# Kernel optimization log

Hardware: AMD Instinct MI355X
Metric: run time of the kernel (lower is better)

Reference implementation:

```python
import jax, jax.numpy as jnp
import numpy as np
from jax import lax

HID = 2048; NK = 16; NV = 32; DK = 128; DV = 128; KSZ = 4; CHUNK = 64; S = 2048
KEY_DIM = NK * DK; VAL_DIM = NV * DV; CONV_DIM = 2 * KEY_DIM + VAL_DIM
EPS = 1e-6


def l2norm(x, eps=1e-6):
    return x * lax.rsqrt((x * x).sum(-1, keepdims=True) + eps)


def chunk_gated_delta_rule(q, k, v, g, beta, chunk=CHUNK):
    # q,k: [B,S,Hv,DK]; v: [B,S,Hv,DV]; g,beta: [B,S,Hv]
    q = l2norm(q); k = l2norm(k)  # use_qk_l2norm_in_kernel=True
    q, k, v = (jnp.swapaxes(x, 1, 2) for x in (q, k, v))  # [B,H,S,D]
    g = jnp.swapaxes(g, 1, 2); beta = jnp.swapaxes(beta, 1, 2)  # [B,H,S]
    B, H, Ssz, Dk = k.shape; Dv = v.shape[-1]
    N = Ssz // chunk  # seq_len chosen divisible by chunk -> pad is no-op
    q = q * (Dk ** -0.5)
    vb = v * beta[..., None]
    kb = k * beta[..., None]
    rs = lambda x: x.reshape(B, H, N, chunk, x.shape[-1])
    q, k, v, kb, vb = map(rs, (q, k, v, kb, vb))
    g = jnp.cumsum(g.reshape(B, H, N, chunk), axis=-1)
    tril = jnp.tril(jnp.ones((chunk, chunk), bool))
    stril = jnp.tril(jnp.ones((chunk, chunk), bool), -1)
    diff = jnp.where(tril, g[..., :, None] - g[..., None, :], 0.0)
    decay_mask = jnp.where(tril, jnp.exp(diff), 0.0)  # [B,H,N,C,C]
    attn = jnp.where(stril, -(kb @ jnp.swapaxes(k, -1, -2)) * decay_mask, 0.0)
    # UT (WY) transform: sequential row updates, scan over in-chunk index
    def ut_body(a, i):
        row = jnp.take(a, i, axis=-2)  # [B,H,N,C]
        new = row + jnp.einsum('bhnk,bhnkj->bhnj', row, a)
        return a.at[:, :, :, i, :].set(new), None
    attn, _ = lax.scan(ut_body, attn, jnp.arange(1, chunk))
    attn = attn + jnp.eye(chunk, dtype=attn.dtype)
    u = attn @ vb                                   # [B,H,N,C,DV]
    kcd = attn @ (kb * jnp.exp(g)[..., None])       # [B,H,N,C,DK]
    init = jnp.zeros((B, H, Dk, Dv), q.dtype)
    def step(state, inp):
        q_i, k_i, u_i, kcd_i, g_i, dm_i = inp
        scores = (q_i @ jnp.swapaxes(k_i, -1, -2)) * dm_i
        v_new = u_i - kcd_i @ state
        inter = (q_i * jnp.exp(g_i)[..., None]) @ state
        o = inter + scores @ v_new
        gl = g_i[..., -1]  # [B,H]
        state = state * jnp.exp(gl)[..., None, None] + jnp.einsum(
            'bhcd,bhce->bhde', k_i * jnp.exp(gl[..., None] - g_i)[..., None], v_new)
        return state, o
    mv = lambda x: jnp.moveaxis(x, 2, 0)
    _, out = lax.scan(step, init, (mv(q), mv(k), mv(u), mv(kcd), mv(g), mv(decay_mask)))
    out = jnp.moveaxis(out, 0, 2).reshape(B, H, Ssz, Dv)
    return jnp.swapaxes(out, 1, 2)  # [B,S,H,DV]


def setup_inputs() -> dict:
    key = jax.random.key(0)
    ks = jax.random.split(key, 8)
    return {
        'hidden_states': jax.random.normal(ks[0], (S, HID), jnp.float32),
        'W_qkv': jax.random.normal(ks[1], (CONV_DIM, HID), jnp.float32) * 0.02,
        'W_z': jax.random.normal(ks[2], (VAL_DIM, HID), jnp.float32) * 0.02,
        'W_a': jax.random.normal(ks[3], (NV, HID), jnp.float32) * 0.02,
        'W_b': jax.random.normal(ks[4], (NV, HID), jnp.float32) * 0.02,
        'conv_w': jax.random.normal(ks[5], (CONV_DIM, 1, KSZ), jnp.float32) * 0.1,
        'dt_bias': jnp.ones((NV,), jnp.float32),
        'A_log': jnp.log(jax.random.uniform(ks[6], (NV,), jnp.float32, 0.1, 16.0)),
        'norm_w': jnp.ones((DV,), jnp.float32),
        'W_out': jax.random.normal(ks[7], (HID, VAL_DIM), jnp.float32) * 0.02,
    }


def reference(hidden_states, W_qkv, W_z, W_a, W_b, conv_w, dt_bias, A_log, norm_w, W_out):
    x = hidden_states  # [S, HID]
    mixed = x @ W_qkv.T  # [S, CONV_DIM]
    z = (x @ W_z.T).reshape(-1, DV)  # [S*NV, DV]
    a = x @ W_a.T  # [S, NV]
    b = x @ W_b.T
    # causal depthwise conv1d (torch pads K-1 both sides then slices [:S])
    conv = lax.conv_general_dilated(
        mixed.T[None], conv_w, (1,), [(KSZ - 1, 0)],
        dimension_numbers=('NCH', 'OIH', 'NCH'), feature_group_count=CONV_DIM)
    mixed = jax.nn.silu(conv[0].T)  # [S, CONV_DIM]
    q = mixed[:, :KEY_DIM].reshape(1, S, NK, DK)
    k = mixed[:, KEY_DIM:2 * KEY_DIM].reshape(1, S, NK, DK)
    v = mixed[:, 2 * KEY_DIM:].reshape(1, S, NV, DV)
    beta = jax.nn.sigmoid(b)[None]  # [1,S,NV]
    g = (-jnp.exp(A_log) * jax.nn.softplus(a + dt_bias))[None]  # [1,S,NV]
    ratio = NV // NK
    q = jnp.repeat(q, ratio, axis=2)
    k = jnp.repeat(k, ratio, axis=2)
    core = chunk_gated_delta_rule(q, k, v, g, beta)  # [1,S,NV,DV]
    h = core.reshape(-1, DV)  # [S*NV, DV]
    var = jnp.mean(h * h, axis=-1, keepdims=True)
    h = h * lax.rsqrt(var + EPS) * norm_w
    h = h * jax.nn.silu(z)
    out = h.reshape(S, VAL_DIM) @ W_out.T  # [S, HID]
    return out
```

## Files before the change

### kernel.cpp

```cpp
#include <hip/hip_runtime.h>
#include <hip/hip_bf16.h>
#include <math.h>

#define S_LEN   2048
#define HIDDIM  2048
#define NKH     16
#define NVH     32
#define DKD     128
#define DVD     128
#define CCH     64
#define NCHK    32
#define KEY_DIM 2048
#define VAL_DIM 4096
#define CONV_DIM 8192

#define PA_LDS_BYTES (16384 + 16384 + 32768 + 4096 + 4096 + 256 + 256 + 256)
#define PB_LDS_BYTES ((8192+8192+4096+8192+2048+1024+1024)*2 + 64*4)
#define G256_LDS_BYTES (3 * 24576 * 2)
#define G128_LDS_BYTES (3 * 16384 * 2)

typedef __bf16 bf16x8 __attribute__((ext_vector_type(8)));
typedef float f32x4 __attribute__((ext_vector_type(4)));

__device__ __forceinline__ float sigmoid_f(float x) { return 1.f / (1.f + __expf(-x)); }
__device__ __forceinline__ float silu_f(float x) { return x * sigmoid_f(x); }
__device__ __forceinline__ ushort f2bf(float f) {
    unsigned u = __float_as_uint(f);
    u += 0x7fffu + ((u >> 16) & 1u);
    return (ushort)(u >> 16);
}
__device__ __forceinline__ float bf2f(ushort u) {
    return __uint_as_float((unsigned)u << 16);
}

#define GLL(srcp, dstp) __builtin_amdgcn_global_load_lds( \
    (const __attribute__((address_space(1))) void*)(srcp), \
    (__attribute__((address_space(3))) void*)(dstp), 16, 0, 0)

__global__ __launch_bounds__(256) void cast_kernel(
    const float* __restrict__ in, ushort* __restrict__ out, int n8)
{
    int t = blockIdx.x * 256 + threadIdx.x;
    if (t >= n8) return;
    float4 v0 = *(const float4*)(in + (size_t)t * 8);
    float4 v1 = *(const float4*)(in + (size_t)t * 8 + 4);
    union { ushort u[8]; uint4 v; } r;
    r.u[0] = f2bf(v0.x); r.u[1] = f2bf(v0.y); r.u[2] = f2bf(v0.z); r.u[3] = f2bf(v0.w);
    r.u[4] = f2bf(v1.x); r.u[5] = f2bf(v1.y); r.u[6] = f2bf(v1.z); r.u[7] = f2bf(v1.w);
    *(uint4*)(out + (size_t)t * 8) = r.v;
}

__global__ __launch_bounds__(256) void cast_ab_kernel(
    const float* __restrict__ Wa, const float* __restrict__ Wb, ushort* __restrict__ out)
{
    int t = blockIdx.x * 256 + threadIdx.x;
    int row = t >> 8;
    int c8 = (t & 255) * 8;
    union { ushort u[8]; uint4 v; } r;
    if (row < 64) {
        const float* src = (row < 32) ? (Wa + (size_t)row * HIDDIM + c8)
                                      : (Wb + (size_t)(row - 32) * HIDDIM + c8);
        float4 v0 = *(const float4*)(src);
        float4 v1 = *(const float4*)(src + 4);
        r.u[0] = f2bf(v0.x); r.u[1] = f2bf(v0.y); r.u[2] = f2bf(v0.z); r.u[3] = f2bf(v0.w);
        r.u[4] = f2bf(v1.x); r.u[5] = f2bf(v1.y); r.u[6] = f2bf(v1.z); r.u[7] = f2bf(v1.w);
    } else {
        r.u[0] = r.u[1] = r.u[2] = r.u[3] = r.u[4] = r.u[5] = r.u[6] = r.u[7] = 0;
    }
    *(uint4*)(out + (size_t)t * 8) = r.v;
}

__global__ __launch_bounds__(512, 2) void gemm256_kernel(
    const ushort* __restrict__ A, const ushort* __restrict__ B,
    float* __restrict__ C0, float* __restrict__ C1,
    int K, int NSPLIT, int ldc0, int ldc1)
{
    extern __shared__ ushort g2s[];
    const int tid = threadIdx.x;
    const int wv = tid >> 6, ln = tid & 63;
    const int wm = wv >> 2, wn = wv & 3;
    const int lrow = ln & 15, lkg = ln >> 4;
    const int bm = blockIdx.y * 128, bn = blockIdx.x * 256;

    int soffA[2], soffB[4];
#pragma unroll
    for (int j = 0; j < 4; ++j) {
        int g = tid + j * 512;
        int frag = g >> 7, ks = (g >> 6) & 1, l = g & 63;
        int off = (frag * 16 + (l & 15)) * K + ks * 32 + (l >> 4) * 8;
        if (j < 2) soffA[j] = off;
        soffB[j] = off;
    }
    const ushort* Abase = A + (size_t)bm * K;
    const ushort* Bbase = B + (size_t)bn * K;

    f32x4 acc[4][4];
#pragma unroll
    for (int m = 0; m < 4; ++m)
#pragma unroll
        for (int n = 0; n < 4; ++n) {
            f32x4 z = {0.f, 0.f, 0.f, 0.f};
            acc[m][n] = z;
        }

#define G256_STAGE(bb, k0) do {                                            \
        ushort* bufA_ = g2s + (bb) * 24576;                                \
        ushort* bufB_ = bufA_ + 8192;                                      \
        _Pragma("unroll")                                                  \
        for (int j_ = 0; j_ < 2; ++j_)                                     \
            GLL(Abase + soffA[j_] + (k0), bufA_ + (j_ * 512 + wv * 64) * 8);\
        _Pragma("unroll")                                                  \
        for (int j_ = 0; j_ < 4; ++j_)                                     \
            GLL(Bbase + soffB[j_] + (k0), bufB_ + (j_ * 512 + wv * 64) * 8);\
    } while (0)

    const int T = K >> 6;
    G256_STAGE(0, 0);
    G256_STAGE(1, 64);
    int bb = 0;
    for (int t = 0; t < T; ++t) {
        if (t + 1 < T) {
            asm volatile("s_waitcnt vmcnt(6)" ::: "memory");
        } else {
            asm volatile("s_waitcnt vmcnt(0)" ::: "memory");
        }
        __builtin_amdgcn_s_barrier();
        if (t + 2 < T) G256_STAGE((bb >= 1) ? (bb - 1) : (bb + 2), (t + 2) * 64);
        const ushort* LA = g2s + bb * 24576;
        const ushort* LB = LA + 8192;
        __builtin_amdgcn_s_setprio(1);
#pragma unroll
        for (int ks = 0; ks < 2; ++ks) {
            bf16x8 afv[4], bfv[4];
#pragma unroll
            for (int mf = 0; mf < 4; ++mf)
                afv[mf] = *(const bf16x8*)&LA[(((wm * 4 + mf) * 2 + ks) * 64 + ln) * 8];
#pragma unroll
            for (int nf = 0; nf < 4; ++nf)
                bfv[nf] = *(const bf16x8*)&LB[(((wn * 4 + nf) * 2 + ks) * 64 + ln) * 8];
#pragma unroll
            for (int mf = 0; mf < 4; ++mf)
#pragma unroll
                for (int nf = 0; nf < 4; ++nf)
                    acc[mf][nf] = __builtin_amdgcn_mfma_f32_16x16x32_bf16(
                        afv[mf], bfv[nf], acc[mf][nf], 0, 0, 0);
        }
        __builtin_amdgcn_s_setprio(0);
        bb = (bb == 2) ? 0 : bb + 1;
    }
#undef G256_STAGE

    const bool inC1 = (bn >= NSPLIT);
    float* Cp = inC1 ? C1 : C0;
    const int ldc = inC1 ? ldc1 : ldc0;
    const int cb = bn + wn * 64 - (inC1 ? NSPLIT : 0);
#pragma unroll
    for (int mf = 0; mf < 4; ++mf) {
        const int row0 = bm + wm * 64 + mf * 16 + lkg * 4;
#pragma unroll
        for (int nf = 0; nf < 4; ++nf) {
            float* cp = Cp + (size_t)row0 * ldc + cb + nf * 16 + lrow;
#pragma unroll
            for (int j = 0; j < 4; ++j) cp[(size_t)j * ldc] = acc[mf][nf][j];
        }
    }
}

__global__ __launch_bounds__(256, 2) void gemm128_kernel(
    const ushort* __restrict__ A, const ushort* __restrict__ B,
    float* __restrict__ C, int N, int K)
{
    extern __shared__ ushort g1s[];
    const int tid = threadIdx.x;
    const int wv = tid >> 6, ln = tid & 63;
    const int wm = wv >> 1, wn = wv & 1;
    const int lrow = ln & 15, lkg = ln >> 4;
    const int bm = blockIdx.y * 128, bn = blockIdx.x * 128;

    int soff[4];
#pragma unroll
    for (int j = 0; j < 4; ++j) {
        int g = tid + j * 256;
        int frag = g >> 7, ks = (g >> 6) & 1, l = g & 63;
        soff[j] = (frag * 16 + (l & 15)) * K + ks * 32 + (l >> 4) * 8;
    }
    const ushort* Abase = A + (size_t)bm * K;
    const ushort* Bbase = B + (size_t)bn * K;

    f32x4 acc[4][4];
#pragma unroll
    for (int m = 0; m < 4; ++m)
#pragma unroll
        for (int n = 0; n < 4; ++n) {
            f32x4 z = {0.f, 0.f, 0.f, 0.f};
            acc[m][n] = z;
        }

#define G128_STAGE(bb, k0) do {                                            \
        ushort* bufA_ = g1s + (bb) * 16384;                                \
        ushort* bufB_ = bufA_ + 8192;                                      \
        _Pragma("unroll")                                                  \
        for (int j_ = 0; j_ < 4; ++j_) {                                   \
            GLL(Abase + soff[j_] + (k0), bufA_ + (j_ * 256 + wv * 64) * 8);\
            GLL(Bbase + soff[j_] + (k0), bufB_ + (j_ * 256 + wv * 64) * 8);\
        }                                                                  \
    } while (0)

    const int T = K >> 6;
    G128_STAGE(0, 0);
    G128_STAGE(1, 64);
    int bb = 0;
    for (int t = 0; t < T; ++t) {
        if (t + 1 < T) {
            asm volatile("s_waitcnt vmcnt(8)" ::: "memory");
        } else {
            asm volatile("s_waitcnt vmcnt(0)" ::: "memory");
        }
        __builtin_amdgcn_s_barrier();
        if (t + 2 < T) G128_STAGE((bb >= 1) ? (bb - 1) : (bb + 2), (t + 2) * 64);
        const ushort* LA = g1s + bb * 16384;
        const ushort* LB = LA + 8192;
        __builtin_amdgcn_s_setprio(1);
#pragma unroll
        for (int ks = 0; ks < 2; ++ks) {
            bf16x8 afv[4], bfv[4];
#pragma unroll
            for (int mf = 0; mf < 4; ++mf)
                afv[mf] = *(const bf16x8*)&LA[(((wm * 4 + mf) * 2 + ks) * 64 + ln) * 8];
#pragma unroll
            for (int nf = 0; nf < 4; ++nf)
                bfv[nf] = *(const bf16x8*)&LB[(((wn * 4 + nf) * 2 + ks) * 64 + ln) * 8];
#pragma unroll
            for (int mf = 0; mf < 4; ++mf)
#pragma unroll
                for (int nf = 0; nf < 4; ++nf)
                    acc[mf][nf] = __builtin_amdgcn_mfma_f32_16x16x32_bf16(
                        afv[mf], bfv[nf], acc[mf][nf], 0, 0, 0);
        }
        __builtin_amdgcn_s_setprio(0);
        bb = (bb == 2) ? 0 : bb + 1;
    }
#undef G128_STAGE

#pragma unroll
    for (int mf = 0; mf < 4; ++mf) {
        const int row0 = bm + wm * 64 + mf * 16 + lkg * 4;
#pragma unroll
        for (int nf = 0; nf < 4; ++nf) {
            float* cp = C + (size_t)row0 * N + bn + wn * 64 + nf * 16 + lrow;
#pragma unroll
            for (int j = 0; j < 4; ++j) cp[(size_t)j * N] = acc[mf][nf][j];
        }
    }
}

__global__ __launch_bounds__(256) void conv_silu_kernel(
    const float* __restrict__ pre, const float* __restrict__ cw, float* __restrict__ out)
{
    int idx = blockIdx.x * 256 + threadIdx.x;
    const int NC4 = CONV_DIM / 4;
    int s = idx / NC4;
    int c = (idx % NC4) * 4;
    float w[4][4];
#pragma unroll
    for (int j = 0; j < 4; ++j) {
        float4 wj = *(const float4*)(cw + (size_t)(c + j) * 4);
        w[j][0] = wj.x; w[j][1] = wj.y; w[j][2] = wj.z; w[j][3] = wj.w;
    }
    float acc[4] = {0.f, 0.f, 0.f, 0.f};
#pragma unroll
    for (int t = 0; t < 4; ++t) {
        int ss = s - 3 + t;
        if (ss >= 0) {
            float4 x = *(const float4*)(pre + (size_t)ss * CONV_DIM + c);
            acc[0] = fmaf(x.x, w[0][t], acc[0]);
            acc[1] = fmaf(x.y, w[1][t], acc[1]);
            acc[2] = fmaf(x.z, w[2][t], acc[2]);
            acc[3] = fmaf(x.w, w[3][t], acc[3]);
        }
    }
    float4 o = make_float4(silu_f(acc[0]), silu_f(acc[1]), silu_f(acc[2]), silu_f(acc[3]));
    *(float4*)(out + (size_t)s * CONV_DIM + c) = o;
}

__global__ __launch_bounds__(256) void gb_kernel(
    const float* __restrict__ ab, const float* __restrict__ dt_bias,
    const float* __restrict__ A_log, float* __restrict__ g, float* __restrict__ beta)
{
    int idx = blockIdx.x * 256 + threadIdx.x;
    int s = idx >> 5, h = idx & 31;
    float av = ab[(size_t)s * 128 + h] + dt_bias[h];
    float sp = (av > 20.f) ? av : log1pf(__expf(av));
    g[idx] = -__expf(A_log[h]) * sp;
    beta[idx] = sigmoid_f(ab[(size_t)s * 128 + 32 + h]);
}

__global__ __launch_bounds__(256) void l2norm_kernel(
    const float* __restrict__ mixed, ushort* __restrict__ qnb, float* __restrict__ kn)
{
    int gw = (blockIdx.x * 256 + threadIdx.x) >> 6;
    int lane = threadIdx.x & 63;
    int isk = gw >= S_LEN * NKH;
    int r = gw - isk * S_LEN * NKH;
    int s = r / NKH, kh = r % NKH;
    const float* src = mixed + (size_t)s * CONV_DIM + isk * KEY_DIM + kh * DKD;
    float2 x = *(const float2*)(src + lane * 2);
    float ss = x.x * x.x + x.y * x.y;
#pragma unroll
    for (int m = 1; m < 64; m <<= 1) ss += __shfl_xor(ss, m, 64);
    float scale = rsqrtf(ss + 1e-6f);
    if (!isk) {
        scale *= 0.08838834764831843f;
        union { ushort u[2]; uint v; } p;
        p.u[0] = f2bf(x.x * scale); p.u[1] = f2bf(x.y * scale);
        *(uint*)(qnb + ((size_t)(s * NKH + kh)) * DKD + lane * 2) = p.v;
    } else {
        float* dst = kn + ((size_t)(s * NKH + kh)) * DKD + lane * 2;
        *(float2*)dst = make_float2(x.x * scale, x.y * scale);
    }
}

__global__ __launch_bounds__(256) void phaseA_kernel(
    const ushort* __restrict__ qnb, const float* __restrict__ kn,
    const float* __restrict__ mixed, const float* __restrict__ gbuf,
    const float* __restrict__ betabuf,
    float* __restrict__ u, ushort* __restrict__ kcd,
    ushort* __restrict__ scores, float* __restrict__ gcs_out,
    ushort* __restrict__ knT)
{
    extern __shared__ char pasm[];
    ushort* kb    = (ushort*)(pasm);
    ushort* qb    = (ushort*)(pasm + 16384);
    ushort* Xb    = (ushort*)(pasm + 32768);
    float*  Adiag = (float*)(pasm + 65536);
    ushort* Ab    = (ushort*)(pasm + 69632);
    float*  gcs_s = (float*)(pasm + 73728);
    float*  bet_s = (float*)(pasm + 73984);
    float*  scK_s = (float*)(pasm + 74240);
    float*  Pf    = (float*)qb;

    const int n = blockIdx.x, h = blockIdx.y, kh = h >> 1;
    const int tid = threadIdx.x;
    const int s0 = n * CCH;
    const int wv = tid >> 6, ln = tid & 63;
    const int lrow = ln & 15, lkg = ln >> 4;

    float xr[64];
    if (tid < 128) {
        const float* vp = mixed + (size_t)s0 * CONV_DIM + 2 * KEY_DIM + h * DVD + tid;
#pragma unroll
        for (int i = 0; i < 64; ++i) xr[i] = vp[(size_t)i * CONV_DIM];
    } else {
        const float* kp = kn + ((size_t)s0 * NKH + kh) * DKD + (tid - 128);
#pragma unroll
        for (int i = 0; i < 64; ++i) xr[i] = kp[(size_t)i * (NKH * DKD)];
    }

    {
        uint4 z = {0, 0, 0, 0};
#pragma unroll
        for (int i = 0; i < 8; ++i)
            *(uint4*)&Xb[(i * 256 + tid) * 8] = z;
        *(uint4*)&Ab[tid * 8] = z;
    }

    if (tid < 64) {
        float gv = gbuf[(size_t)(s0 + tid) * NVH + h];
#pragma unroll
        for (int off = 1; off < 64; off <<= 1) {
            float pv = __shfl_up(gv, off, 64);
            if (tid >= off) gv += pv;
        }
        float bv = betabuf[(size_t)(s0 + tid) * NVH + h];
        gcs_s[tid] = gv;
        bet_s[tid] = bv;
        scK_s[tid] = bv * __expf(gv);
        gcs_out[(size_t)h * S_LEN + s0 + tid] = gv;
    }

    {
        const int r = tid >> 2, c0 = (tid & 3) * 32;
        const int mbase = (((r >> 4) * 4 + (tid & 3)) * 64 + (r & 15)) * 8;
        const float* ksrc = kn + ((size_t)(s0 + r) * NKH + kh) * DKD + c0;
#pragma unroll
        for (int j0 = 0; j0 < 4; ++j0) {
            float4 v0 = *(const float4*)(ksrc + j0 * 8);
            float4 v1 = *(const float4*)(ksrc + j0 * 8 + 4);
            union { ushort us[8]; uint4 v; } p;
            p.us[0] = f2bf(v0.x); p.us[1] = f2bf(v0.y); p.us[2] = f2bf(v0.z); p.us[3] = f2bf(v0.w);
            p.us[4] = f2bf(v1.x); p.us[5] = f2bf(v1.y); p.us[6] = f2bf(v1.z); p.us[7] = f2bf(v1.w);
            *(uint4*)&kb[mbase + (j0 << 7)] = p.v;
        }
        const ushort* qsrc = qnb + ((size_t)(s0 + r) * NKH + kh) * DKD + c0;
#pragma unroll
        for (int j0 = 0; j0 < 4; ++j0) {
            uint4 v = *(const uint4*)(qsrc + j0 * 8);
            *(uint4*)&qb[mbase + (j0 << 7)] = v;
        }
    }
    __syncthreads();

    f32x4 accA[4], accQ[4];
#pragma unroll
    for (int j = 0; j < 4; ++j) {
        f32x4 z = {0.f, 0.f, 0.f, 0.f};
        accA[j] = z; accQ[j] = z;
    }
#pragma unroll
    for (int ks = 0; ks < 4; ++ks) {
        bf16x8 a_k = *(const bf16x8*)&kb[((wv * 4 + ks) * 64 + ln) * 8];
        bf16x8 a_q = *(const bf16x8*)&qb[((wv * 4 + ks) * 64 + ln) * 8];
#pragma unroll
        for (int j = 0; j < 4; ++j) {
            bf16x8 b_k = *(const bf16x8*)&kb[((j * 4 + ks) * 64 + ln) * 8];
            accA[j] = __builtin_amdgcn_mfma_f32_16x16x32_bf16(a_k, b_k, accA[j], 0, 0, 0);
            accQ[j] = __builtin_amdgcn_mfma_f32_16x16x32_bf16(a_q, b_k, accQ[j], 0, 0, 0);
        }
    }
    {
        ushort* scp = scores + (size_t)(h * NCHK + n) * (CCH * CCH);
#pragma unroll
        for (int j = 0; j < 4; ++j) {
            const int c = j * 16 + lrow;
            const float gc = gcs_s[c];
#pragma unroll
            for (int jj = 0; jj < 4; ++jj) {
                const int i = wv * 16 + lkg * 4 + jj;
                const float e = __expf(gcs_s[i] - gc);
                float sv = (i >= c) ? (accQ[j][jj] * e) : 0.f;
                scp[i * CCH + c] = f2bf(sv);
                float aval = (i > c) ? (-bet_s[i] * accA[j][jj] * e) : 0.f;
                if (j == wv) {
                    Adiag[wv * 256 + (i & 15) * 16 + lrow] = aval;
                } else if (j < wv) {
                    const int f = (wv == 1) ? 0 : ((wv == 2) ? 1 : (2 + (j >> 1)));
                    const int lk = ((j & 1) << 4) | lrow;
                    const int lane2 = (i & 15) | ((lk >> 3) << 4);
                    Ab[(f * 64 + lane2) * 8 + (lk & 7)] = f2bf(aval);
                }
            }
        }
    }
    if (tid < 128) {
#pragma unroll
        for (int i4 = 0; i4 < 16; ++i4) {
            float4 b4 = *(const float4*)&bet_s[i4 * 4];
            xr[i4 * 4 + 0] *= b4.x; xr[i4 * 4 + 1] *= b4.y;
            xr[i4 * 4 + 2] *= b4.z; xr[i4 * 4 + 3] *= b4.w;
        }
    } else {
#pragma unroll
        for (int i4 = 0; i4 < 16; ++i4) {
            float4 b4 = *(const float4*)&scK_s[i4 * 4];
            xr[i4 * 4 + 0] *= b4.x; xr[i4 * 4 + 1] *= b4.y;
            xr[i4 * 4 + 2] *= b4.z; xr[i4 * 4 + 3] *= b4.w;
        }
    }
    __syncthreads();

    const int ct = tid >> 4, lct = tid & 15;
#pragma unroll
    for (int s = 0; s < 4; ++s) {
        float y[16];
        float pr[16];
        if (s > 0) {
#pragma unroll
            for (int r = 0; r < 16; ++r) pr[r] = Pf[r * 256 + tid];
        } else {
#pragma unroll
            for (int r = 0; r < 16; ++r) pr[r] = 0.f;
        }
#pragma unroll
        for (int r = 0; r < 16; ++r) {
            float acc = xr[s * 16 + r] + pr[r];
#pragma unroll
            for (int k4 = 0; k4 < 16; k4 += 4) {
                if (k4 < r) {
                    float4 a4 = *(const float4*)&Adiag[s * 256 + r * 16 + k4];
                    if (k4 + 0 < r) acc = fmaf(a4.x, y[k4 + 0], acc);
                    if (k4 + 1 < r) acc = fmaf(a4.y, y[k4 + 1], acc);
                    if (k4 + 2 < r) acc = fmaf(a4.z, y[k4 + 2], acc);
                    if (k4 + 3 < r) acc = fmaf(a4.w, y[k4 + 3], acc);
                }
            }
            y[r] = acc;
        }
        if (tid < 128) {
            float* up = u + (size_t)(h * NCHK + n) * (CCH * DVD) + (s * 16) * DVD + tid;
#pragma unroll
            for (int r = 0; r < 16; ++r) up[r * DVD] = y[r];
        } else {
            ushort* kp = kcd + (size_t)(h * NCHK + n) * (CCH * DKD) + (s * 16) * DKD + (tid - 128);
#pragma unroll
            for (int r = 0; r < 16; ++r) kp[r * DKD] = f2bf(y[r]);
        }
        if (s < 3) {
#pragma unroll
            for (int half = 0; half < 2; ++half) {
                union { ushort us[8]; uint4 v; } p;
#pragma unroll
                for (int e = 0; e < 8; ++e) p.us[e] = f2bf(y[half * 8 + e]);
                const int kg = (s & 1) * 2 + half;
                *(uint4*)&Xb[(((s >> 1) * 16 + ct) * 64 + (kg * 16 + lct)) * 8] = p.v;
            }
            __syncthreads();
            const int snx = s + 1;
            const int nT2 = (snx + 1) >> 1;
            f32x4 accP[4];
#pragma unroll
            for (int ctl = 0; ctl < 4; ++ctl) {
                f32x4 z = {0.f, 0.f, 0.f, 0.f};
                accP[ctl] = z;
            }
#pragma unroll
            for (int t2 = 0; t2 < 2; ++t2) {
                if (t2 < nT2) {
                    const int f = (snx == 1) ? 0 : ((snx == 2) ? 1 : (2 + t2));
                    bf16x8 a = *(const bf16x8*)&Ab[(f * 64 + ln) * 8];
#pragma unroll
                    for (int ctl = 0; ctl < 4; ++ctl) {
                        bf16x8 b = *(const bf16x8*)&Xb[((t2 * 16 + wv * 4 + ctl) * 64 + ln) * 8];
                        accP[ctl] = __builtin_amdgcn_mfma_f32_16x16x32_bf16(a, b, accP[ctl], 0, 0, 0);
                    }
                }
            }
#pragma unroll
            for (int ctl = 0; ctl < 4; ++ctl)
#pragma unroll
                for (int jj = 0; jj < 4; ++jj)
                    Pf[(lkg * 4 + jj) * 256 + wv * 64 + ctl * 16 + lrow] = accP[ctl][jj];
            __syncthreads();
        }
    }

    if (!(h & 1)) {
        const int dk = tid >> 1, ch = (tid & 1) * 32;
        ushort* dst = knT + ((size_t)(kh * NCHK + n) * DKD + dk) * CCH + ch;
        const int kpart = ((dk >> 5) * 64) * 8 + (((dk >> 3) & 3) << 4) * 8 + (dk & 7);
#pragma unroll
        for (int j0 = 0; j0 < 32; j0 += 8) {
            union { ushort us[8]; uint4 v; } p;
#pragma unroll
            for (int j = 0; j < 8; ++j) {
                const int row = ch + j0 + j;
                p.us[j] = kb[((row >> 4) * 4 * 64 + (row & 15)) * 8 + kpart];
            }
            *(uint4*)(dst + j0) = p.v;
        }
    }
}

__global__ __launch_bounds__(256) void phaseB_kernel(
    const ushort* __restrict__ qnb, const ushort* __restrict__ knT,
    const float* __restrict__ u, const ushort* __restrict__ kcd,
    const ushort* __restrict__ sc, const float* __restrict__ gcs,
    float* __restrict__ obuf)
{
    extern __shared__ ushort smu[];
    ushort* qorg  = smu;
    ushort* kcorg = smu + 8192;
    ushort* scorg = smu + 16384;
    ushort* kTorg = smu + 20480;
    ushort* storg = smu + 28672;
    ushort* vnorg = smu + 30720;
    ushort* vnsorg= smu + 31744;
    float* gcs_s  = (float*)(smu + 32768);

    const int h = blockIdx.x;
    const int dvb = blockIdx.y;
    const int d0 = dvb * 16;
    const int kh = h >> 1;
    const int tid = threadIdx.x;
    const int wv = tid >> 6, ln = tid & 63;
    const int lrow = ln & 15, lkg = ln >> 4;

    for (int i = tid; i < 2048 / 8; i += 256) {
        uint4 z = {0, 0, 0, 0};
        *(uint4*)&storg[i * 8] = z;
    }

    const int q_lane  = lrow * (NKH * DKD) + kh * DKD + wv * 32 + lkg * 8;
    const int kc_lane = lrow * DKD + wv * 32 + lkg * 8;
    const int st_lane = ((tid >> 7) * 16 + lrow) * 64 + ((tid >> 6) & 1) * 32 + lkg * 8;
    const int dst_e   = wv * 512;

    f32x4 accS0 = {0.f, 0.f, 0.f, 0.f}, accS1 = {0.f, 0.f, 0.f, 0.f};

    for (int n = 0; n < NCHK; ++n) {
        const int s0 = n * CCH;
        const ushort* qsrc  = qnb + (size_t)s0 * (NKH * DKD);
        const ushort* kcsrc = kcd + (size_t)(h * NCHK + n) * (CCH * DKD);
        const ushort* scsrc = sc  + (size_t)(h * NCHK + n) * (CCH * CCH);
        const ushort* kTsrc = knT + (size_t)(kh * NCHK + n) * (DKD * CCH);
#pragma unroll
        for (int r = 0; r < 4; ++r) {
            GLL(qsrc + q_lane + r * 32768, &qorg[r * 2048 + dst_e]);
            GLL(kcsrc + kc_lane + r * 2048, &kcorg[r * 2048 + dst_e]);
            GLL(kTsrc + st_lane + r * 2048, &kTorg[r * 2048 + dst_e]);
        }
#pragma unroll
        for (int r = 0; r < 2; ++r)
            GLL(scsrc + st_lane + r * 2048, &scorg[r * 2048 + dst_e]);
        if (tid < 64) gcs_s[tid] = gcs[(size_t)h * S_LEN + s0 + tid];
        __syncthreads();

        f32x4 accv = {0.f, 0.f, 0.f, 0.f};
        f32x4 acco = {0.f, 0.f, 0.f, 0.f};
#pragma unroll
        for (int ks = 0; ks < 4; ++ks) {
            bf16x8 b_st = *(const bf16x8*)&storg[(ks * 64 + ln) * 8];
            bf16x8 a_kc = *(const bf16x8*)&kcorg[((wv * 4 + ks) * 64 + ln) * 8];
            bf16x8 a_q  = *(const bf16x8*)&qorg[((wv * 4 + ks) * 64 + ln) * 8];
            accv = __builtin_amdgcn_mfma_f32_16x16x32_bf16(a_kc, b_st, accv, 0, 0, 0);
            acco = __builtin_amdgcn_mfma_f32_16x16x32_bf16(a_q, b_st, acco, 0, 0, 0);
        }
        const float* up = u + (size_t)(h * NCHK + n) * (CCH * DVD)
                            + (wv * 16 + lkg * 4) * DVD + d0 + lrow;
        float u0 = up[0], u1 = up[DVD], u2 = up[2 * DVD], u3 = up[3 * DVD];
        const float gl = gcs_s[63];
        float vn0 = u0 - accv[0], vn1 = u1 - accv[1];
        float vn2 = u2 - accv[2], vn3 = u3 - accv[3];
        {
            const int row = wv * 16 + lkg * 4;
            float g0 = gcs_s[row], g1 = gcs_s[row + 1], g2 = gcs_s[row + 2], g3 = gcs_s[row + 3];
            acco[0] *= __expf(g0); acco[1] *= __expf(g1);
            acco[2] *= __expf(g2); acco[3] *= __expf(g3);
            const int eb = ((wv >> 1) * 64 + ((wv & 1) * 2 + (lkg >> 1)) * 16 + lrow) * 8
                         + (lkg & 1) * 4;
            union { ushort u2a[4]; uint2 v; } pa, pb;
            pa.u2a[0] = f2bf(vn0); pa.u2a[1] = f2bf(vn1);
            pa.u2a[2] = f2bf(vn2); pa.u2a[3] = f2bf(vn3);
            pb.u2a[0] = f2bf(vn0 * __expf(gl - g0)); pb.u2a[1] = f2bf(vn1 * __expf(gl - g1));
            pb.u2a[2] = f2bf(vn2 * __expf(gl - g2)); pb.u2a[3] = f2bf(vn3 * __expf(gl - g3));
            *(uint2*)&vnorg[eb] = pa.v;
            *(uint2*)&vnsorg[eb] = pb.v;
        }
        __syncthreads();

#pragma unroll
        for (int ks = 0; ks < 2; ++ks) {
            bf16x8 a_sc = *(const bf16x8*)&scorg[((wv * 2 + ks) * 64 + ln) * 8];
            bf16x8 b_vn = *(const bf16x8*)&vnorg[(ks * 64 + ln) * 8];
            acco = __builtin_amdgcn_mfma_f32_16x16x32_bf16(a_sc, b_vn, acco, 0, 0, 0);
        }
        float* op = obuf + (size_t)(s0 + wv * 16 + lkg * 4) * VAL_DIM + h * DVD + d0 + lrow;
        op[0] = acco[0]; op[VAL_DIM] = acco[1];
        op[2 * VAL_DIM] = acco[2]; op[3 * VAL_DIM] = acco[3];

        const float egl = __expf(gl);
        accS0 *= egl; accS1 *= egl;
#pragma unroll
        for (int ks = 0; ks < 2; ++ks) {
            bf16x8 a_vs = *(const bf16x8*)&vnsorg[(ks * 64 + ln) * 8];
            bf16x8 b_k0 = *(const bf16x8*)&kTorg[(((wv * 2 + 0) * 2 + ks) * 64 + ln) * 8];
            bf16x8 b_k1 = *(const bf16x8*)&kTorg[(((wv * 2 + 1) * 2 + ks) * 64 + ln) * 8];
            accS0 = __builtin_amdgcn_mfma_f32_16x16x32_bf16(a_vs, b_k0, accS0, 0, 0, 0);
            accS1 = __builtin_amdgcn_mfma_f32_16x16x32_bf16(a_vs, b_k1, accS1, 0, 0, 0);
        }
#pragma unroll
        for (int j = 0; j < 4; ++j) {
            storg[(wv * 64 + ((lrow >> 3)) * 16 + lkg * 4 + j) * 8 + (lrow & 7)] = f2bf(accS0[j]);
            storg[(wv * 64 + (2 + (lrow >> 3)) * 16 + lkg * 4 + j) * 8 + (lrow & 7)] = f2bf(accS1[j]);
        }
        __syncthreads();
    }
}

__global__ __launch_bounds__(256) void norm_kernel(
    const float* __restrict__ obuf, const float* __restrict__ z,
    const float* __restrict__ nw, ushort* __restrict__ hbuf)
{
    int row = (blockIdx.x * 256 + threadIdx.x) >> 6;
    int lane = threadIdx.x & 63;
    float2 x = *(const float2*)(obuf + (size_t)row * DVD + lane * 2);
    float ss = x.x * x.x + x.y * x.y;
#pragma unroll
    for (int m = 1; m < 64; m <<= 1) ss += __shfl_xor(ss, m, 64);
    float scale = rsqrtf(ss * (1.f / DVD) + 1e-6f);
    float2 zz = *(const float2*)(z + (size_t)row * DVD + lane * 2);
    float2 w2 = *(const float2*)(nw + lane * 2);
    float h0 = x.x * scale * w2.x * silu_f(zz.x);
    float h1 = x.y * scale * w2.y * silu_f(zz.y);
    union { ushort u[2]; uint v; } r;
    r.u[0] = f2bf(h0); r.u[1] = f2bf(h1);
    *(uint*)(hbuf + (size_t)row * DVD + lane * 2) = r.v;
}

extern "C" void kernel_launch(void* const* d_in, const int* in_sizes, int n_in,
                              void* d_out, int out_size, void* d_ws, size_t ws_size,
                              hipStream_t stream)
{
    (void)in_sizes; (void)n_in; (void)out_size; (void)ws_size;
    const float* x      = (const float*)d_in[0];
    const float* W_qkv  = (const float*)d_in[1];
    const float* W_z    = (const float*)d_in[2];
    const float* W_a    = (const float*)d_in[3];
    const float* W_b    = (const float*)d_in[4];
    const float* conv_w = (const float*)d_in[5];
    const float* dt_b   = (const float*)d_in[6];
    const float* A_log  = (const float*)d_in[7];
    const float* norm_w = (const float*)d_in[8];
    const float* W_out  = (const float*)d_in[9];
    float* out = (float*)d_out;

    char* ws = (char*)d_ws;
    float*  mixed_pre = (float*)(ws);
    float*  u_buf     = (float*)(ws);
    ushort* kcd_buf   = (ushort*)(ws + 33554432);
    ushort* knT_buf   = (ushort*)(ws + 50331648);
    ushort* wqz       = (ushort*)(ws + 67108864);
    ushort* xb        = (ushort*)(ws + 117440512);
    float*  mixed     = (float*)(ws + 67108864);
    float*  obuf      = (float*)(ws + 67108864);
    ushort* hbuf      = (ushort*)(ws + 100663296);
    ushort* wob       = (ushort*)(ws + 117440512);
    float*  z_buf     = (float*)(ws + 134217728);
    ushort* sc_buf    = (ushort*)(ws + 167772160);
    ushort* wabb      = (ushort*)(ws + 167772160);
    float*  ab_buf    = (float*)(ws + 168296448);
    ushort* qnb       = (ushort*)(ws + 176160768);
    float*  kn        = (float*)(ws + 184549376);
    float*  g_buf     = (float*)(ws + 201326592);
    float*  bet_buf   = (float*)(ws + 201588736);
    float*  gcs_buf   = (float*)(ws + 201850880);

    hipFuncSetAttribute((const void*)phaseA_kernel,
                        hipFuncAttributeMaxDynamicSharedMemorySize, PA_LDS_BYTES);
    hipFuncSetAttribute((const void*)phaseB_kernel,
                        hipFuncAttributeMaxDynamicSharedMemorySize, PB_LDS_BYTES);
    hipFuncSetAttribute((const void*)gemm256_kernel,
                        hipFuncAttributeMaxDynamicSharedMemorySize, G256_LDS_BYTES);
    hipFuncSetAttribute((const void*)gemm128_kernel,
                        hipFuncAttributeMaxDynamicSharedMemorySize, G128_LDS_BYTES);

    dim3 blk(256);
    cast_kernel<<<(S_LEN * HIDDIM / 8) / 256, blk, 0, stream>>>(x, xb, S_LEN * HIDDIM / 8);
    cast_kernel<<<(CONV_DIM * HIDDIM / 8) / 256, blk, 0, stream>>>(W_qkv, wqz, CONV_DIM * HIDDIM / 8);
    cast_kernel<<<(VAL_DIM * HIDDIM / 8) / 256, blk, 0, stream>>>(W_z, wqz + (size_t)CONV_DIM * HIDDIM, VAL_DIM * HIDDIM / 8);
    cast_ab_kernel<<<(128 * HIDDIM / 8) / 256, blk, 0, stream>>>(W_a, W_b, wabb);
    gemm256_kernel<<<dim3((CONV_DIM + VAL_DIM) / 256, S_LEN / 128), dim3(512), G256_LDS_BYTES, stream>>>(
        xb, wqz, mixed_pre, z_buf, HIDDIM, CONV_DIM, CONV_DIM, VAL_DIM);
    gemm128_kernel<<<dim3(1, S_LEN / 128), blk, G128_LDS_BYTES, stream>>>(
        xb, wabb, ab_buf, 128, HIDDIM);
    conv_silu_kernel<<<(S_LEN * CONV_DIM / 4) / 256, blk, 0, stream>>>(mixed_pre, conv_w, mixed);
    gb_kernel<<<(S_LEN * NVH) / 256, blk, 0, stream>>>(ab_buf, dt_b, A_log, g_buf, bet_buf);
    l2norm_kernel<<<(2 * S_LEN * NKH * 64) / 256, blk, 0, stream>>>(mixed, qnb, kn);
    phaseA_kernel<<<dim3(NCHK, NVH), blk, PA_LDS_BYTES, stream>>>(
        qnb, kn, mixed, g_buf, bet_buf, u_buf, kcd_buf, sc_buf, gcs_buf, knT_buf);
    phaseB_kernel<<<dim3(NVH, 8), blk, PB_LDS_BYTES, stream>>>(
        qnb, knT_buf, u_buf, kcd_buf, sc_buf, gcs_buf, obuf);
    cast_kernel<<<(HIDDIM * VAL_DIM / 8) / 256, blk, 0, stream>>>(W_out, wob, HIDDIM * VAL_DIM / 8);
    norm_kernel<<<(S_LEN * NVH * 64) / 256, blk, 0, stream>>>(obuf, z_buf, norm_w, hbuf);
    gemm128_kernel<<<dim3(HIDDIM / 128, S_LEN / 128), blk, G128_LDS_BYTES, stream>>>(
        hbuf, wob, out, HIDDIM, VAL_DIM);
}
```

Before: 491.7 us.

## Replace 128x256 projection GEMM with 256x256 eight-phase ping-pong pipelined kernel

The large input projection GEMM moves from 128x256 tiles with a 3-stage buffer to 256x256 tiles with two 64 KB LDS buffers. The K loop is split into eight phases that interleave partial global-to-LDS loads with MFMA sub-blocks under barriers. This doubles reuse of each loaded B tile and overlaps memory traffic with compute. The cost is 128 KB of LDS per block, twice the accumulator registers, more barriers, and half as many blocks (384), which may hurt occupancy and wave balance across CUs.

```diff
diff --git a/kernel.cpp b/kernel.cpp
--- a/kernel.cpp
+++ b/kernel.cpp
@@ -16,7 +16,7 @@
 
 #define PA_LDS_BYTES (16384 + 16384 + 32768 + 4096 + 4096 + 256 + 256 + 256)
 #define PB_LDS_BYTES ((8192+8192+4096+8192+2048+1024+1024)*2 + 64*4)
-#define G256_LDS_BYTES (3 * 24576 * 2)
+#define G8P_LDS_BYTES (2 * 65536)
 #define G128_LDS_BYTES (3 * 16384 * 2)
 
 typedef __bf16 bf16x8 __attribute__((ext_vector_type(8)));
@@ -70,93 +70,223 @@
     *(uint4*)(out + (size_t)t * 8) = r.v;
 }
 
-__global__ __launch_bounds__(512, 2) void gemm256_kernel(
+__global__ __launch_bounds__(512, 2) void gemm8p_kernel(
     const ushort* __restrict__ A, const ushort* __restrict__ B,
     float* __restrict__ C0, float* __restrict__ C1,
     int K, int NSPLIT, int ldc0, int ldc1)
 {
-    extern __shared__ ushort g2s[];
+    extern __shared__ ushort g8s[];
     const int tid = threadIdx.x;
     const int wv = tid >> 6, ln = tid & 63;
     const int wm = wv >> 2, wn = wv & 3;
     const int lrow = ln & 15, lkg = ln >> 4;
-    const int bm = blockIdx.y * 128, bn = blockIdx.x * 256;
-
-    int soffA[2], soffB[4];
-#pragma unroll
-    for (int j = 0; j < 4; ++j) {
-        int g = tid + j * 512;
-        int frag = g >> 7, ks = (g >> 6) & 1, l = g & 63;
-        int off = (frag * 16 + (l & 15)) * K + ks * 32 + (l >> 4) * 8;
-        if (j < 2) soffA[j] = off;
-        soffB[j] = off;
-    }
-    const ushort* Abase = A + (size_t)bm * K;
-    const ushort* Bbase = B + (size_t)bn * K;
-
-    f32x4 acc[4][4];
-#pragma unroll
-    for (int m = 0; m < 4; ++m)
+    const int bm = blockIdx.y * 256, bn = blockIdx.x * 256;
+
+    int soff[4];
+#pragma unroll
+    for (int g = 0; g < 4; ++g) {
+        int gr = g * 512 + tid;
+        int frag = gr >> 7, ks = (gr >> 6) & 1, l = gr & 63;
+        soff[g] = (frag * 16 + (l & 15)) * K + ks * 32 + (l >> 4) * 8;
+    }
+    const ushort* Ag = A + (size_t)bm * K;
+    const ushort* Bg = B + (size_t)bn * K;
+
+#define STG_A(bsel, g, kk) GLL(Ag + soff[g] + (kk), \
+        g8s + (bsel) * 32768 + ((g) * 512 + wv * 64) * 8)
+#define STG_B(bsel, g, kk) GLL(Bg + soff[g] + (kk), \
+        g8s + (bsel) * 32768 + 16384 + ((g) * 512 + wv * 64) * 8)
+#define BARX() do { asm volatile("" ::: "memory"); __builtin_amdgcn_s_barrier(); } while (0)
+#define VMW(n) asm volatile("s_waitcnt vmcnt(" #n ")" ::: "memory")
+
+    f32x4 acc[8][4];
+#pragma unroll
+    for (int m = 0; m < 8; ++m)
 #pragma unroll
         for (int n = 0; n < 4; ++n) {
             f32x4 z = {0.f, 0.f, 0.f, 0.f};
             acc[m][n] = z;
         }
 
-#define G256_STAGE(bb, k0) do {                                            \
-        ushort* bufA_ = g2s + (bb) * 24576;                                \
-        ushort* bufB_ = bufA_ + 8192;                                      \
-        _Pragma("unroll")                                                  \
-        for (int j_ = 0; j_ < 2; ++j_)                                     \
-            GLL(Abase + soffA[j_] + (k0), bufA_ + (j_ * 512 + wv * 64) * 8);\
-        _Pragma("unroll")                                                  \
-        for (int j_ = 0; j_ < 4; ++j_)                                     \
-            GLL(Bbase + soffB[j_] + (k0), bufB_ + (j_ * 512 + wv * 64) * 8);\
-    } while (0)
-
-    const int T = K >> 6;
-    G256_STAGE(0, 0);
-    G256_STAGE(1, 64);
-    int bb = 0;
-    for (int t = 0; t < T; ++t) {
-        if (t + 1 < T) {
-            asm volatile("s_waitcnt vmcnt(6)" ::: "memory");
-        } else {
-            asm volatile("s_waitcnt vmcnt(0)" ::: "memory");
-        }
-        __builtin_amdgcn_s_barrier();
-        if (t + 2 < T) G256_STAGE((bb >= 1) ? (bb - 1) : (bb + 2), (t + 2) * 64);
-        const ushort* LA = g2s + bb * 24576;
-        const ushort* LB = LA + 8192;
+    const ushort* LA0 = g8s;
+    const ushort* LB0 = g8s + 16384;
+    const ushort* LA1 = g8s + 32768;
+    const ushort* LB1 = g8s + 49152;
+
+#pragma unroll
+    for (int g = 0; g < 4; ++g) STG_A(0, g, 0);
+#pragma unroll
+    for (int g = 0; g < 4; ++g) STG_B(0, g, 0);
+    STG_A(1, 0, 64); STG_A(1, 1, 64);
+    VMW(2);
+    BARX();
+
+    const int T2 = K >> 7;
+    for (int it = 0; it < T2; ++it) {
+        const int kc = it * 128;
+        const bool more = (it + 1 < T2);
+        bf16x8 a[4][2], b0[2][2], b1[2][2];
+
+#pragma unroll
+        for (int mf = 0; mf < 4; ++mf)
+#pragma unroll
+            for (int ks = 0; ks < 2; ++ks)
+                a[mf][ks] = *(const bf16x8*)&LA0[(((wm * 8 + mf) * 2 + ks) * 64 + ln) * 8];
+#pragma unroll
+        for (int nf = 0; nf < 2; ++nf)
+#pragma unroll
+            for (int ks = 0; ks < 2; ++ks)
+                b0[nf][ks] = *(const bf16x8*)&LB0[(((wn * 4 + nf) * 2 + ks) * 64 + ln) * 8];
+        STG_A(1, 2, kc + 64); STG_A(1, 3, kc + 64);
+        BARX();
         __builtin_amdgcn_s_setprio(1);
 #pragma unroll
-        for (int ks = 0; ks < 2; ++ks) {
-            bf16x8 afv[4], bfv[4];
-#pragma unroll
-            for (int mf = 0; mf < 4; ++mf)
-                afv[mf] = *(const bf16x8*)&LA[(((wm * 4 + mf) * 2 + ks) * 64 + ln) * 8];
-#pragma unroll
-            for (int nf = 0; nf < 4; ++nf)
-                bfv[nf] = *(const bf16x8*)&LB[(((wn * 4 + nf) * 2 + ks) * 64 + ln) * 8];
-#pragma unroll
-            for (int mf = 0; mf < 4; ++mf)
-#pragma unroll
-                for (int nf = 0; nf < 4; ++nf)
+        for (int mf = 0; mf < 4; ++mf)
+#pragma unroll
+            for (int nf = 0; nf < 2; ++nf)
+#pragma unroll
+                for (int ks = 0; ks < 2; ++ks)
                     acc[mf][nf] = __builtin_amdgcn_mfma_f32_16x16x32_bf16(
-                        afv[mf], bfv[nf], acc[mf][nf], 0, 0, 0);
-        }
+                        a[mf][ks], b0[nf][ks], acc[mf][nf], 0, 0, 0);
         __builtin_amdgcn_s_setprio(0);
-        bb = (bb == 2) ? 0 : bb + 1;
-    }
-#undef G256_STAGE
+        BARX();
+#pragma unroll
+        for (int nf = 0; nf < 2; ++nf)
+#pragma unroll
+            for (int ks = 0; ks < 2; ++ks)
+                b1[nf][ks] = *(const bf16x8*)&LB0[(((wn * 4 + 2 + nf) * 2 + ks) * 64 + ln) * 8];
+        STG_B(1, 0, kc + 64); STG_B(1, 1, kc + 64);
+        BARX();
+        __builtin_amdgcn_s_setprio(1);
+#pragma unroll
+        for (int mf = 0; mf < 4; ++mf)
+#pragma unroll
+            for (int nf = 0; nf < 2; ++nf)
+#pragma unroll
+                for (int ks = 0; ks < 2; ++ks)
+                    acc[mf][2 + nf] = __builtin_amdgcn_mfma_f32_16x16x32_bf16(
+                        a[mf][ks], b1[nf][ks], acc[mf][2 + nf], 0, 0, 0);
+        __builtin_amdgcn_s_setprio(0);
+        BARX();
+#pragma unroll
+        for (int mf = 0; mf < 4; ++mf)
+#pragma unroll
+            for (int ks = 0; ks < 2; ++ks)
+                a[mf][ks] = *(const bf16x8*)&LA0[(((wm * 8 + 4 + mf) * 2 + ks) * 64 + ln) * 8];
+        STG_B(1, 2, kc + 64); STG_B(1, 3, kc + 64);
+        BARX();
+        __builtin_amdgcn_s_setprio(1);
+#pragma unroll
+        for (int mf = 0; mf < 4; ++mf)
+#pragma unroll
+            for (int nf = 0; nf < 2; ++nf)
+#pragma unroll
+                for (int ks = 0; ks < 2; ++ks)
+                    acc[4 + mf][nf] = __builtin_amdgcn_mfma_f32_16x16x32_bf16(
+                        a[mf][ks], b0[nf][ks], acc[4 + mf][nf], 0, 0, 0);
+        __builtin_amdgcn_s_setprio(0);
+        BARX();
+        if (more) { STG_A(0, 0, kc + 128); STG_A(0, 1, kc + 128); }
+        BARX();
+        __builtin_amdgcn_s_setprio(1);
+#pragma unroll
+        for (int mf = 0; mf < 4; ++mf)
+#pragma unroll
+            for (int nf = 0; nf < 2; ++nf)
+#pragma unroll
+                for (int ks = 0; ks < 2; ++ks)
+                    acc[4 + mf][2 + nf] = __builtin_amdgcn_mfma_f32_16x16x32_bf16(
+                        a[mf][ks], b1[nf][ks], acc[4 + mf][2 + nf], 0, 0, 0);
+        __builtin_amdgcn_s_setprio(0);
+        if (more) { VMW(2); } else { VMW(0); }
+        BARX();
+
+#pragma unroll
+        for (int mf = 0; mf < 4; ++mf)
+#pragma unroll
+            for (int ks = 0; ks < 2; ++ks)
+                a[mf][ks] = *(const bf16x8*)&LA1[(((wm * 8 + mf) * 2 + ks) * 64 + ln) * 8];
+#pragma unroll
+        for (int nf = 0; nf < 2; ++nf)
+#pragma unroll
+            for (int ks = 0; ks < 2; ++ks)
+                b0[nf][ks] = *(const bf16x8*)&LB1[(((wn * 4 + nf) * 2 + ks) * 64 + ln) * 8];
+        if (more) { STG_A(0, 2, kc + 128); STG_A(0, 3, kc + 128); }
+        BARX();
+        __builtin_amdgcn_s_setprio(1);
+#pragma unroll
+        for (int mf = 0; mf < 4; ++mf)
+#pragma unroll
+            for (int nf = 0; nf < 2; ++nf)
+#pragma unroll
+                for (int ks = 0; ks < 2; ++ks)
+                    acc[mf][nf] = __builtin_amdgcn_mfma_f32_16x16x32_bf16(
+                        a[mf][ks], b0[nf][ks], acc[mf][nf], 0, 0, 0);
+        __builtin_amdgcn_s_setprio(0);
+        BARX();
+#pragma unroll
+        for (int nf = 0; nf < 2; ++nf)
+#pragma unroll
+            for (int ks = 0; ks < 2; ++ks)
+                b1[nf][ks] = *(const bf16x8*)&LB1[(((wn * 4 + 2 + nf) * 2 + ks) * 64 + ln) * 8];
+        if (more) { STG_B(0, 0, kc + 128); STG_B(0, 1, kc + 128); }
+        BARX();
+        __builtin_amdgcn_s_setprio(1);
+#pragma unroll
+        for (int mf = 0; mf < 4; ++mf)
+#pragma unroll
+            for (int nf = 0; nf < 2; ++nf)
+#pragma unroll
+                for (int ks = 0; ks < 2; ++ks)
+                    acc[mf][2 + nf] = __builtin_amdgcn_mfma_f32_16x16x32_bf16(
+                        a[mf][ks], b1[nf][ks], acc[mf][2 + nf], 0, 0, 0);
+        __builtin_amdgcn_s_setprio(0);
+        BARX();
+#pragma unroll
+        for (int mf = 0; mf < 4; ++mf)
+#pragma unroll
+            for (int ks = 0; ks < 2; ++ks)
+                a[mf][ks] = *(const bf16x8*)&LA1[(((wm * 8 + 4 + mf) * 2 + ks) * 64 + ln) * 8];
+        if (more) { STG_B(0, 2, kc + 128); STG_B(0, 3, kc + 128); }
+        BARX();
+        __builtin_amdgcn_s_setprio(1);
+#pragma unroll
+        for (int mf = 0; mf < 4; ++mf)
+#pragma unroll
+            for (int nf = 0; nf < 2; ++nf)
+#pragma unroll
+                for (int ks = 0; ks < 2; ++ks)
+                    acc[4 + mf][nf] = __builtin_amdgcn_mfma_f32_16x16x32_bf16(
+                        a[mf][ks], b0[nf][ks], acc[4 + mf][nf], 0, 0, 0);
+        __builtin_amdgcn_s_setprio(0);
+        BARX();
+        if (more) { STG_A(1, 0, kc + 192); STG_A(1, 1, kc + 192); }
+        BARX();
+        __builtin_amdgcn_s_setprio(1);
+#pragma unroll
+        for (int mf = 0; mf < 4; ++mf)
+#pragma unroll
+            for (int nf = 0; nf < 2; ++nf)
+#pragma unroll
+                for (int ks = 0; ks < 2; ++ks)
+                    acc[4 + mf][2 + nf] = __builtin_amdgcn_mfma_f32_16x16x32_bf16(
+                        a[mf][ks], b1[nf][ks], acc[4 + mf][2 + nf], 0, 0, 0);
+        __builtin_amdgcn_s_setprio(0);
+        VMW(2);
+        BARX();
+    }
+#undef STG_A
+#undef STG_B
+#undef BARX
+#undef VMW
 
     const bool inC1 = (bn >= NSPLIT);
     float* Cp = inC1 ? C1 : C0;
     const int ldc = inC1 ? ldc1 : ldc0;
     const int cb = bn + wn * 64 - (inC1 ? NSPLIT : 0);
 #pragma unroll
-    for (int mf = 0; mf < 4; ++mf) {
-        const int row0 = bm + wm * 64 + mf * 16 + lkg * 4;
+    for (int mf = 0; mf < 8; ++mf) {
+        const int row0 = bm + wm * 128 + mf * 16 + lkg * 4;
 #pragma unroll
         for (int nf = 0; nf < 4; ++nf) {
             float* cp = Cp + (size_t)row0 * ldc + cb + nf * 16 + lrow;
@@ -728,8 +858,8 @@
                         hipFuncAttributeMaxDynamicSharedMemorySize, PA_LDS_BYTES);
     hipFuncSetAttribute((const void*)phaseB_kernel,
                         hipFuncAttributeMaxDynamicSharedMemorySize, PB_LDS_BYTES);
-    hipFuncSetAttribute((const void*)gemm256_kernel,
-                        hipFuncAttributeMaxDynamicSharedMemorySize, G256_LDS_BYTES);
+    hipFuncSetAttribute((const void*)gemm8p_kernel,
+                        hipFuncAttributeMaxDynamicSharedMemorySize, G8P_LDS_BYTES);
     hipFuncSetAttribute((const void*)gemm128_kernel,
                         hipFuncAttributeMaxDynamicSharedMemorySize, G128_LDS_BYTES);
 
@@ -738,7 +868,7 @@
     cast_kernel<<<(CONV_DIM * HIDDIM / 8) / 256, blk, 0, stream>>>(W_qkv, wqz, CONV_DIM * HIDDIM / 8);
     cast_kernel<<<(VAL_DIM * HIDDIM / 8) / 256, blk, 0, stream>>>(W_z, wqz + (size_t)CONV_DIM * HIDDIM, VAL_DIM * HIDDIM / 8);
     cast_ab_kernel<<<(128 * HIDDIM / 8) / 256, blk, 0, stream>>>(W_a, W_b, wabb);
-    gemm256_kernel<<<dim3((CONV_DIM + VAL_DIM) / 256, S_LEN / 128), dim3(512), G256_LDS_BYTES, stream>>>(
+    gemm8p_kernel<<<dim3((CONV_DIM + VAL_DIM) / 256, S_LEN / 256), dim3(512), G8P_LDS_BYTES, stream>>>(
         xb, wqz, mixed_pre, z_buf, HIDDIM, CONV_DIM, CONV_DIM, VAL_DIM);
     gemm128_kernel<<<dim3(1, S_LEN / 128), blk, G128_LDS_BYTES, stream>>>(
         xb, wabb, ab_buf, 128, HIDDIM);
```

Result: slower. 596.1 us (+21.2%).
